# Kernel optimization log

Hardware: AMD Instinct MI355X
Metric: run time of the kernel (lower is better)

Reference implementation:

```python
import jax, jax.numpy as jnp
import numpy as np

C = 768
H = 12
N = 257
B = 64
HID = 4 * C
EPS = 1e-5
SCALE = (C // H) ** -0.5


def layer_norm(x, g, b):
    m = x.mean(-1, keepdims=True)
    v = ((x - m) ** 2).mean(-1, keepdims=True)
    return (x - m) * jax.lax.rsqrt(v + EPS) * g + b


def qkv_split(x, qkv_w):
    # x: [B,N,C]; qkv_w: [3C,C] (torch Linear layout)
    qkv = jnp.einsum('bnc,oc->bno', x, qkv_w)  # [B,N,3C]
    qkv = qkv.reshape(x.shape[0], x.shape[1], 3, H, C // H)
    qkv = jnp.transpose(qkv, (2, 0, 3, 1, 4))  # [3,B,H,N,hd]
    return qkv[0], qkv[1], qkv[2]


def self_attn(x, qkv_w, proj_w, proj_b):
    q, k, v = qkv_split(x, qkv_w)
    attn = jax.nn.softmax(jnp.einsum('bhnd,bhmd->bhnm', q, k) * SCALE, axis=-1)
    o = jnp.einsum('bhnm,bhmd->bhnd', attn, v)
    o = jnp.transpose(o, (0, 2, 1, 3)).reshape(x.shape)
    return jnp.einsum('bnc,oc->bno', o, proj_w) + proj_b


def cross_attn(x, y, qkv_w, proj_w, proj_b):
    qx, _, _ = qkv_split(x, qkv_w)
    _, ky, vy = qkv_split(y, qkv_w)
    attn = jax.nn.softmax(jnp.einsum('bhnd,bhmd->bhnm', qx, ky) * SCALE, axis=-1)
    o = jnp.einsum('bhnm,bhmd->bhnd', attn, vy)
    o = jnp.transpose(o, (0, 2, 1, 3)).reshape(x.shape)
    return jnp.einsum('bnc,oc->bno', o, proj_w) + proj_b, attn.sum(1)  # [B,N,N]


def mlp(x, w1, b1, w2, b2):
    h = jax.nn.gelu(jnp.einsum('bnc,hc->bnh', x, w1) + b1, approximate=False)
    return jnp.einsum('bnh,ch->bnc', h, w2) + b2


def arf(x):
    tmp = (jnp.exp(x) - jnp.exp(-x)) / (jnp.exp(x) + jnp.exp(-x - 4.0))
    return jnp.where(tmp < 0, jnp.zeros_like(x), tmp)


def setup_inputs() -> dict:
    key = jax.random.key(0)
    ks = jax.random.split(key, 16)
    s = 0.02
    return {
        'src': jax.random.normal(ks[0], (B, N, C), jnp.float32),
        'tgt': jax.random.normal(ks[1], (B, N, C), jnp.float32),
        'sattn_qkv_w': jax.random.normal(ks[2], (3 * C, C), jnp.float32) * s,
        'sattn_proj_w': jax.random.normal(ks[3], (C, C), jnp.float32) * s,
        'sattn_proj_b': jnp.zeros((C,), jnp.float32),
        'cattn_qkv_w': jax.random.normal(ks[4], (3 * C, C), jnp.float32) * s,
        'cattn_proj_w': jax.random.normal(ks[5], (C, C), jnp.float32) * s,
        'cattn_proj_b': jnp.zeros((C,), jnp.float32),
        'norm1_g': jnp.ones((C,), jnp.float32),
        'norm1_b': jnp.zeros((C,), jnp.float32),
        'norm2_g': jnp.ones((C,), jnp.float32),
        'norm2_b': jnp.zeros((C,), jnp.float32),
        'fc1_w': jax.random.normal(ks[6], (HID, C), jnp.float32) * s,
        'fc1_b': jnp.zeros((HID,), jnp.float32),
        'fc2_w': jax.random.normal(ks[7], (C, HID), jnp.float32) * s,
        'fc2_b': jnp.zeros((C,), jnp.float32),
        'sa_weight': jnp.ones((1, 1, C), jnp.float32),
        'pos_embed': jax.random.normal(ks[8], (1, N, C), jnp.float32) * s,
    }


def reference(src, tgt, sattn_qkv_w, sattn_proj_w, sattn_proj_b,
              cattn_qkv_w, cattn_proj_w, cattn_proj_b,
              norm1_g, norm1_b, norm2_g, norm2_b,
              fc1_w, fc1_b, fc2_w, fc2_b, sa_weight, pos_embed):
    src = src + pos_embed
    srct = self_attn(layer_norm(src, norm1_g, norm1_b), sattn_qkv_w, sattn_proj_w, sattn_proj_b)
    tgtt = self_attn(layer_norm(tgt, norm1_g, norm1_b), sattn_qkv_w, sattn_proj_w, sattn_proj_b)
    src = src + srct
    tgt = tgt + tgtt
    src = src + mlp(layer_norm(srct, norm2_g, norm2_b), fc1_w, fc1_b, fc2_w, fc2_b)
    tgt = tgt + mlp(layer_norm(tgtt, norm2_g, norm2_b), fc1_w, fc1_b, fc2_w, fc2_b)
    srct, attn_src = cross_attn(layer_norm(src, norm1_g, norm1_b),
                                layer_norm(tgt, norm1_g, norm1_b),
                                cattn_qkv_w, cattn_proj_w, cattn_proj_b)
    srct = arf(srct)
    src = src + srct
    src = src + mlp(layer_norm(srct, norm2_g, norm2_b), fc1_w, fc1_b, fc2_w, fc2_b)
    attm_out = attn_src[:, 1:, 1:]
    # heat gate (no grad through attn_src here)
    heat = jax.lax.stop_gradient(attn_src)
    heat = heat.mean(1).reshape(attn_src.shape[0], N, 1)  # [B,N,1]
    gate = jax.nn.sigmoid(heat)
    tgt = tgt + tgt * sa_weight * gate
    return src, tgt, attm_out
```

## Files before the change

### kernel.cpp

```cpp
#include <hip/hip_runtime.h>

#define N_SEQ  257
#define BATCH  64
#define CDIM   768
#define HEADS  12
#define HDIM   64
#define HIDDEN 3072
#define MROWS  (BATCH * N_SEQ)

typedef unsigned short u16;
typedef unsigned int   u32;
typedef __bf16 bf16x8 __attribute__((ext_vector_type(8)));
typedef float  f32x4  __attribute__((ext_vector_type(4)));

__device__ __forceinline__ float b2f(u16 u) { u32 x = ((u32)u) << 16; return __uint_as_float(x); }
__device__ __forceinline__ u16   f2b(float f) {
    u32 x = __float_as_uint(f);
    u32 r = (x + 0x7fffu + ((x >> 16) & 1u)) >> 16;
    return (u16)r;
}
__device__ __forceinline__ float ldf(const float x) { return x; }
__device__ __forceinline__ float ldf(const u16 x)   { return b2f(x); }

__device__ __forceinline__ float geluf(float x) { return 0.5f * x * (1.f + erff(x * 0.70710678118654752f)); }
__device__ __forceinline__ float arff(float x) {
    if (x <= 0.f) return 0.f;
    float a = expf(-2.f * x);
    float c = expf(-2.f * x - 4.f);
    return (1.f - a) / (1.f + c);
}

template<bool MAXOP>
__device__ __forceinline__ float block_red(float v, float* scratch, int tid) {
#pragma unroll
    for (int off = 32; off > 0; off >>= 1) {
        float o = __shfl_down(v, off, 64);
        v = MAXOP ? fmaxf(v, o) : v + o;
    }
    if ((tid & 63) == 0) scratch[tid >> 6] = v;
    __syncthreads();
    float r = MAXOP ? fmaxf(fmaxf(scratch[0], scratch[1]), fmaxf(scratch[2], scratch[3]))
                    : (scratch[0] + scratch[1]) + (scratch[2] + scratch[3]);
    __syncthreads();
    return r;
}

__global__ void detect_kernel(const u16* __restrict__ g1, u32* __restrict__ flag)
{
    if (threadIdx.x == 0 && blockIdx.x == 0) *flag = (g1[0] == 0x3F80u) ? 1u : 0u;
}

__global__ __launch_bounds__(256)
void conv_kernel(const void* __restrict__ s, u16* __restrict__ d, int n,
                 const u32* __restrict__ flag)
{
    const int i = blockIdx.x * 256 + threadIdx.x;
    if (i >= n) return;
    if (*flag) d[i] = ((const u16*)s)[i];
    else       d[i] = f2b(((const float*)s)[i]);
}

#define LDSW 40

template<int EP>
__global__ __launch_bounds__(256)
void gemm_kernel(const u16* __restrict__ A, const u16* __restrict__ W,
                 const u16* __restrict__ bias, u16* __restrict__ Co,
                 float* __restrict__ resid, int M, int Ncols, int K)
{
    __shared__ __align__(16) u16 sA[128 * LDSW];
    __shared__ __align__(16) u16 sB[128 * LDSW];
    const int tid  = threadIdx.x;
    const int bm0  = blockIdx.y * 128;
    const int n0   = blockIdx.x * 128;
    const int lane = tid & 63, wave = tid >> 6;
    const int wm = (wave >> 1) << 6;
    const int wn = (wave & 1) << 6;
    const int r16 = lane & 15, quad = lane >> 4;

    f32x4 acc[4][4] = {};

    for (int k0 = 0; k0 < K; k0 += 32) {
        __syncthreads();
#pragma unroll
        for (int it = 0; it < 2; ++it) {
            int c2  = tid + (it << 8);
            int row = c2 >> 2;
            int col = (c2 & 3) << 3;
            int gm  = bm0 + row; if (gm >= M) gm = M - 1;
            *reinterpret_cast<uint4*>(&sA[row * LDSW + col]) =
                *reinterpret_cast<const uint4*>(A + (size_t)gm * K + k0 + col);
            *reinterpret_cast<uint4*>(&sB[row * LDSW + col]) =
                *reinterpret_cast<const uint4*>(W + (size_t)(n0 + row) * K + k0 + col);
        }
        __syncthreads();

        bf16x8 af[4], bfr[4];
#pragma unroll
        for (int i = 0; i < 4; ++i) {
            af[i]  = *reinterpret_cast<const bf16x8*>(&sA[(wm + i * 16 + r16) * LDSW + quad * 8]);
            bfr[i] = *reinterpret_cast<const bf16x8*>(&sB[(wn + i * 16 + r16) * LDSW + quad * 8]);
        }
#pragma unroll
        for (int i = 0; i < 4; ++i)
#pragma unroll
            for (int j = 0; j < 4; ++j)
                acc[i][j] = __builtin_amdgcn_mfma_f32_16x16x32_bf16(af[i], bfr[j], acc[i][j], 0, 0, 0);
    }

#pragma unroll
    for (int i = 0; i < 4; ++i) {
#pragma unroll
        for (int j = 0; j < 4; ++j) {
            const int gn = n0 + wn + j * 16 + r16;
            const float bv = bias ? b2f(bias[gn]) : 0.f;
#pragma unroll
            for (int r = 0; r < 4; ++r) {
                const int gm = bm0 + wm + i * 16 + quad * 4 + r;
                if (gm < M) {
                    float v = acc[i][j][r] + bv;
                    const size_t oidx = (size_t)gm * Ncols + gn;
                    if (EP == 1) v = geluf(v);
                    if (EP == 3) v = arff(v);
                    if (EP == 0 || EP == 1) Co[oidx] = f2b(v);
                    if (EP == 2 || EP == 3) { Co[oidx] = f2b(v); resid[oidx] += v; }
                    if (EP == 4) resid[oidx] += v;
                }
            }
        }
    }
}

template<typename T>
__global__ __launch_bounds__(256)
void ln_kernel(const T* __restrict__ x, const u16* __restrict__ g,
               const u16* __restrict__ be, u16* __restrict__ y)
{
    __shared__ float scratch[4];
    const int row = blockIdx.x, tid = threadIdx.x;
    const size_t base = (size_t)row * CDIM;
    float v[3];
#pragma unroll
    for (int i = 0; i < 3; ++i) v[i] = ldf(x[base + tid + i * 256]);
    float mean = block_red<false>(v[0] + v[1] + v[2], scratch, tid) * (1.f / 768.f);
    float d0 = v[0] - mean, d1 = v[1] - mean, d2 = v[2] - mean;
    float var = block_red<false>(d0 * d0 + d1 * d1 + d2 * d2, scratch, tid) * (1.f / 768.f);
    float rstd = rsqrtf(var + 1e-5f);
#pragma unroll
    for (int i = 0; i < 3; ++i) {
        int c = tid + i * 256;
        y[base + c] = f2b((v[i] - mean) * rstd * b2f(g[c]) + b2f(be[c]));
    }
}

__global__ __launch_bounds__(256, 4)
void attn_flash_kernel(const u16* __restrict__ Q, int qs,
                       const u16* __restrict__ Kp, int ks,
                       const u16* __restrict__ Vp, int vs,
                       u16* __restrict__ O,
                       float* __restrict__ Mg, float* __restrict__ Ig)
{
    __shared__ __align__(16) u16 Vt[2][64 * 64];
    __shared__ __align__(16) u16 Ps[64 * 72];
    const int tid = threadIdx.x;
    const int n0 = blockIdx.x * 64;
    const int h  = blockIdx.y, b = blockIdx.z;
    const int lane = tid & 63, w = tid >> 6;
    const int r16 = lane & 15, quad = lane >> 4;

    int qrow = n0 + w * 16 + r16; if (qrow > 256) qrow = 256;
    const u16* qp = Q + (size_t)(b * N_SEQ + qrow) * qs + h * HDIM + quad * 8;
    const bf16x8 af0 = *reinterpret_cast<const bf16x8*>(qp);
    const bf16x8 af1 = *reinterpret_cast<const bf16x8*>(qp + 32);

    auto stageV = [&](int kt, int buf) {
#pragma unroll
        for (int it = 0; it < 2; ++it) {
            int id  = tid + (it << 8);
            int key = id & 63;
            int dc  = ((id >> 6) & 7) << 3;
            int gm  = kt * 64 + key; if (gm > 256) gm = 256;
            uint4 v4 = *reinterpret_cast<const uint4*>(Vp + (size_t)(b * N_SEQ + gm) * vs + h * HDIM + dc);
            const u16* vv = reinterpret_cast<const u16*>(&v4);
#pragma unroll
            for (int j = 0; j < 8; ++j) {
                int d = dc + j;
                Vt[buf][d * 64 + (key ^ ((d & 7) << 3))] = vv[j];
            }
        }
    };

    f32x4 O4[4];
#pragma unroll
    for (int s = 0; s < 4; ++s) O4[s] = (f32x4){0.f, 0.f, 0.f, 0.f};
    float m_[4] = { -3.0e38f, -3.0e38f, -3.0e38f, -3.0e38f };
    float l_[4] = { 0.f, 0.f, 0.f, 0.f };

    stageV(0, 0);
    __syncthreads();

    for (int kt = 0; kt < 5; ++kt) {
        if (kt < 4) stageV(kt + 1, (kt + 1) & 1);

        f32x4 s4[4];
#pragma unroll
        for (int s = 0; s < 4; ++s) s4[s] = (f32x4){0.f, 0.f, 0.f, 0.f};
#pragma unroll
        for (int s = 0; s < 4; ++s) {
            int krow = kt * 64 + s * 16 + r16; if (krow > 256) krow = 256;
            const u16* kp = Kp + (size_t)(b * N_SEQ + krow) * ks + h * HDIM + quad * 8;
            bf16x8 b0 = *reinterpret_cast<const bf16x8*>(kp);
            bf16x8 b1 = *reinterpret_cast<const bf16x8*>(kp + 32);
            s4[s] = __builtin_amdgcn_mfma_f32_16x16x32_bf16(af0, b0, s4[s], 0, 0, 0);
            s4[s] = __builtin_amdgcn_mfma_f32_16x16x32_bf16(af1, b1, s4[s], 0, 0, 0);
        }

#pragma unroll
        for (int s = 0; s < 4; ++s)
#pragma unroll
            for (int r = 0; r < 4; ++r) {
                float v = s4[s][r] * 0.125f;
                if (kt == 4 && (s * 16 + r16) >= 1) v = -3.0e38f;
                s4[s][r] = v;
            }

#pragma unroll
        for (int r = 0; r < 4; ++r) {
            float tmax = fmaxf(fmaxf(s4[0][r], s4[1][r]), fmaxf(s4[2][r], s4[3][r]));
#pragma unroll
            for (int msk = 1; msk < 16; msk <<= 1) tmax = fmaxf(tmax, __shfl_xor(tmax, msk, 64));
            float mn = fmaxf(m_[r], tmax);
            float corr = __expf(m_[r] - mn);
            m_[r] = mn;
            float rs = 0.f;
#pragma unroll
            for (int s = 0; s < 4; ++s) {
                float p = __expf(s4[s][r] - mn);
                s4[s][r] = p; rs += p;
            }
#pragma unroll
            for (int msk = 1; msk < 16; msk <<= 1) rs += __shfl_xor(rs, msk, 64);
            l_[r] = l_[r] * corr + rs;
#pragma unroll
            for (int s = 0; s < 4; ++s) O4[s][r] *= corr;
        }

#pragma unroll
        for (int ts = 0; ts < 4; ++ts)
#pragma unroll
            for (int r = 0; r < 4; ++r)
                Ps[(w * 16 + quad * 4 + r) * 72 + ts * 16 + r16] = f2b(s4[ts][r]);
        bf16x8 p0 = *reinterpret_cast<const bf16x8*>(&Ps[(w * 16 + r16) * 72 + quad * 8]);
        bf16x8 p1 = *reinterpret_cast<const bf16x8*>(&Ps[(w * 16 + r16) * 72 + 32 + quad * 8]);
#pragma unroll
        for (int s = 0; s < 4; ++s) {
            const int d0 = s * 16 + r16;
            const int sw = (d0 & 7) << 3;
            bf16x8 v0 = *reinterpret_cast<const bf16x8*>(&Vt[kt & 1][d0 * 64 + ((quad * 8) ^ sw)]);
            bf16x8 v1 = *reinterpret_cast<const bf16x8*>(&Vt[kt & 1][d0 * 64 + ((32 + quad * 8) ^ sw)]);
            O4[s] = __builtin_amdgcn_mfma_f32_16x16x32_bf16(p0, v0, O4[s], 0, 0, 0);
            O4[s] = __builtin_amdgcn_mfma_f32_16x16x32_bf16(p1, v1, O4[s], 0, 0, 0);
        }

        __syncthreads();
    }

    float inv[4];
#pragma unroll
    for (int r = 0; r < 4; ++r) inv[r] = 1.f / l_[r];

    if (Mg) {
#pragma unroll
        for (int r = 0; r < 4; ++r) {
            const int n = n0 + w * 16 + quad * 4 + r;
            if (r16 == 0 && n < N_SEQ) {
                const size_t mi = (size_t)(b * HEADS + h) * N_SEQ + n;
                Mg[mi] = m_[r]; Ig[mi] = inv[r];
            }
        }
    }

#pragma unroll
    for (int s = 0; s < 4; ++s) {
#pragma unroll
        for (int r = 0; r < 4; ++r) {
            const int n = n0 + w * 16 + quad * 4 + r;
            if (n < N_SEQ)
                O[(size_t)(b * N_SEQ + n) * CDIM + h * HDIM + s * 16 + r16] = f2b(O4[s][r] * inv[r]);
        }
    }
}

__global__ __launch_bounds__(256, 2)
void asum_kernel(const u16* __restrict__ Q, int qs,
                 const u16* __restrict__ Kp, int ks,
                 const float* __restrict__ Mg, const float* __restrict__ Ig,
                 float* __restrict__ asum)
{
    const int tid = threadIdx.x;
    const int n0 = blockIdx.x * 64;
    const int b  = blockIdx.y;
    const int lane = tid & 63, w = tid >> 6;
    const int r16 = lane & 15, quad = lane >> 4;

    f32x4 A00 = {0.f,0.f,0.f,0.f}, A01 = {0.f,0.f,0.f,0.f}, A02 = {0.f,0.f,0.f,0.f}, A03 = {0.f,0.f,0.f,0.f};
    f32x4 A10 = {0.f,0.f,0.f,0.f}, A11 = {0.f,0.f,0.f,0.f}, A12 = {0.f,0.f,0.f,0.f}, A13 = {0.f,0.f,0.f,0.f};
    f32x4 A20 = {0.f,0.f,0.f,0.f}, A21 = {0.f,0.f,0.f,0.f}, A22 = {0.f,0.f,0.f,0.f}, A23 = {0.f,0.f,0.f,0.f};
    f32x4 A30 = {0.f,0.f,0.f,0.f}, A31 = {0.f,0.f,0.f,0.f}, A32 = {0.f,0.f,0.f,0.f}, A33 = {0.f,0.f,0.f,0.f};
    f32x4 A40 = {0.f,0.f,0.f,0.f}, A41 = {0.f,0.f,0.f,0.f}, A42 = {0.f,0.f,0.f,0.f}, A43 = {0.f,0.f,0.f,0.f};

    for (int h = 0; h < HEADS; ++h) {
        int qrow = n0 + w * 16 + r16; if (qrow > 256) qrow = 256;
        const u16* qp = Q + (size_t)(b * N_SEQ + qrow) * qs + h * HDIM + quad * 8;
        const bf16x8 af0 = *reinterpret_cast<const bf16x8*>(qp);
        const bf16x8 af1 = *reinterpret_cast<const bf16x8*>(qp + 32);

        float mv[4], iv[4];
#pragma unroll
        for (int r = 0; r < 4; ++r) {
            int n = n0 + w * 16 + quad * 4 + r; if (n > 256) n = 256;
            const size_t mi = (size_t)(b * HEADS + h) * N_SEQ + n;
            mv[r] = Mg[mi]; iv[r] = Ig[mi];
        }

#define ASUM_TS(KT, S, AV) { \
        int krow = KT * 64 + S * 16 + r16; if (krow > 256) krow = 256; \
        const u16* kp = Kp + (size_t)(b * N_SEQ + krow) * ks + h * HDIM + quad * 8; \
        bf16x8 b0 = *reinterpret_cast<const bf16x8*>(kp); \
        bf16x8 b1 = *reinterpret_cast<const bf16x8*>(kp + 32); \
        f32x4 t = (f32x4){0.f, 0.f, 0.f, 0.f}; \
        t = __builtin_amdgcn_mfma_f32_16x16x32_bf16(af0, b0, t, 0, 0, 0); \
        t = __builtin_amdgcn_mfma_f32_16x16x32_bf16(af1, b1, t, 0, 0, 0); \
        _Pragma("unroll") \
        for (int r = 0; r < 4; ++r) { \
            float p = __expf(t[r] * 0.125f - mv[r]) * iv[r]; \
            if (KT == 4 && (S * 16 + r16) >= 1) p = 0.f; \
            AV[r] += p; \
        } }

        ASUM_TS(0, 0, A00) ASUM_TS(0, 1, A01) ASUM_TS(0, 2, A02) ASUM_TS(0, 3, A03)
        ASUM_TS(1, 0, A10) ASUM_TS(1, 1, A11) ASUM_TS(1, 2, A12) ASUM_TS(1, 3, A13)
        ASUM_TS(2, 0, A20) ASUM_TS(2, 1, A21) ASUM_TS(2, 2, A22) ASUM_TS(2, 3, A23)
        ASUM_TS(3, 0, A30) ASUM_TS(3, 1, A31) ASUM_TS(3, 2, A32) ASUM_TS(3, 3, A33)
        ASUM_TS(4, 0, A40) ASUM_TS(4, 1, A41) ASUM_TS(4, 2, A42) ASUM_TS(4, 3, A43)
#undef ASUM_TS
    }

#define ASUM_ST(KT, S, AV) { \
    _Pragma("unroll") \
    for (int r = 0; r < 4; ++r) { \
        const int n = n0 + w * 16 + quad * 4 + r; \
        const int key = KT * 64 + S * 16 + r16; \
        if (n < N_SEQ && key < N_SEQ) \
            asum[((size_t)b * N_SEQ + n) * N_SEQ + key] = AV[r]; \
    } }

    ASUM_ST(0, 0, A00) ASUM_ST(0, 1, A01) ASUM_ST(0, 2, A02) ASUM_ST(0, 3, A03)
    ASUM_ST(1, 0, A10) ASUM_ST(1, 1, A11) ASUM_ST(1, 2, A12) ASUM_ST(1, 3, A13)
    ASUM_ST(2, 0, A20) ASUM_ST(2, 1, A21) ASUM_ST(2, 2, A22) ASUM_ST(2, 3, A23)
    ASUM_ST(3, 0, A30) ASUM_ST(3, 1, A31) ASUM_ST(3, 2, A32) ASUM_ST(3, 3, A33)
    ASUM_ST(4, 0, A40) ASUM_ST(4, 1, A41) ASUM_ST(4, 2, A42) ASUM_ST(4, 3, A43)
#undef ASUM_ST
}

__global__ __launch_bounds__(256)
void init_kernel(const void* __restrict__ src, const void* __restrict__ tgt,
                 const void* __restrict__ pos, float* __restrict__ sa,
                 float* __restrict__ ta, const u32* __restrict__ flag)
{
    const u32 i = blockIdx.x * 256 + threadIdx.x;
    const u32 p = i % (u32)(N_SEQ * CDIM);
    float sv, tv, pv;
    if (*flag) {
        sv = b2f(((const u16*)src)[i]); tv = b2f(((const u16*)tgt)[i]); pv = b2f(((const u16*)pos)[p]);
    } else {
        sv = ((const float*)src)[i];    tv = ((const float*)tgt)[i];    pv = ((const float*)pos)[p];
    }
    sa[i] = sv + pv;
    ta[i] = tv;
}

__global__ __launch_bounds__(256)
void gate_kernel(const float* __restrict__ asum, float* __restrict__ gate)
{
    const int b = blockIdx.x;
    for (int m = threadIdx.x; m < N_SEQ; m += 256) {
        float s = 0.f;
        for (int q = 0; q < N_SEQ; ++q)
            s += asum[((size_t)b * N_SEQ + q) * N_SEQ + m];
        s *= (1.f / 257.f);
        gate[b * N_SEQ + m] = 1.f / (1.f + expf(-s));
    }
}

__global__ __launch_bounds__(256)
void final_kernel(const float* __restrict__ sa, const float* __restrict__ ta,
                  const u16* __restrict__ saw, const float* __restrict__ gate,
                  void* __restrict__ osrc_v, const u32* __restrict__ flag)
{
    const u32 i = blockIdx.x * 256 + threadIdx.x;
    const int c  = i % CDIM;
    const int bn = i / CDIM;
    const float so = sa[i];
    const float to = ta[i] * (1.f + b2f(saw[c]) * gate[bn]);
    const size_t BNC = (size_t)MROWS * CDIM;
    if (*flag) {
        u16* o = (u16*)osrc_v;
        o[i] = f2b(so); o[BNC + i] = f2b(to);
    } else {
        float* o = (float*)osrc_v;
        o[i] = so; o[BNC + i] = to;
    }
}

__global__ __launch_bounds__(256)
void attm_kernel(const float* __restrict__ asum, void* __restrict__ out_v,
                 const u32* __restrict__ flag)
{
    const u32 i = blockIdx.x * 256 + threadIdx.x;
    const int b = i >> 16;
    const int r = (i >> 8) & 255;
    const int c = i & 255;
    const float v = asum[((size_t)b * N_SEQ + (r + 1)) * N_SEQ + (c + 1)];
    const size_t off = 2 * (size_t)MROWS * CDIM;
    if (*flag) ((u16*)out_v)[off + i] = f2b(v);
    else       ((float*)out_v)[off + i] = v;
}

extern "C" void kernel_launch(void* const* d_in, const int* in_sizes, int n_in,
                              void* d_out, int out_size, void* d_ws, size_t ws_size,
                              hipStream_t stream)
{
    const void* src    = d_in[0];
    const void* tgt    = d_in[1];
    const void* pos    = d_in[17];

    const int M = MROWS;
    const size_t BNC = (size_t)M * CDIM;

    float* SA   = (float*)d_ws;
    float* TA   = SA + BNC;
    u16*   Cb   = (u16*)(TA + BNC);
    u16*   Db   = Cb + BNC;
    u16*   Eb   = Db + BNC;
    float* ASUM = (float*)(Eb + 4 * BNC);
    float* GATE = ASUM + (size_t)BATCH * N_SEQ * N_SEQ;
    u16*   WB   = (u16*)(GATE + (size_t)BATCH * N_SEQ);
    u16* w_sqkv   = WB;
    u16* w_sproj  = w_sqkv  + 1769472;
    u16* w_sprojb = w_sproj + 589824;
    u16* w_cqkv   = w_sprojb + 768;
    u16* w_cproj  = w_cqkv  + 1769472;
    u16* w_cprojb = w_cproj + 589824;
    u16* w_g1     = w_cprojb + 768;
    u16* w_b1     = w_g1 + 768;
    u16* w_g2     = w_b1 + 768;
    u16* w_b2     = w_g2 + 768;
    u16* w_fc1    = w_b2 + 768;
    u16* w_fc1b   = w_fc1 + 2359296;
    u16* w_fc2    = w_fc1b + 3072;
    u16* w_fc2b   = w_fc2 + 2359296;
    u16* w_saw    = w_fc2b + 768;
    u32* FLAG     = (u32*)(w_saw + 768);
    const size_t NMI = (size_t)BATCH * HEADS * N_SEQ;
    float* MG     = (float*)(FLAG + 4);
    float* IG     = MG + NMI;
    if (ws_size < (size_t)((char*)(IG + NMI) - (char*)d_ws)) return;

    const dim3 blk(256, 1, 1);
    const int gM = (M + 127) / 128;
    const dim3 agrid(5, HEADS, BATCH);

    detect_kernel<<<dim3(1), dim3(64), 0, stream>>>((const u16*)d_in[8], FLAG);

    auto conv = [&](int idx, u16* dst, int n) {
        conv_kernel<<<dim3((n + 255) / 256), blk, 0, stream>>>(d_in[idx], dst, n, FLAG);
    };
    conv(2,  w_sqkv,   1769472);
    conv(3,  w_sproj,  589824);
    conv(4,  w_sprojb, 768);
    conv(5,  w_cqkv,   1769472);
    conv(6,  w_cproj,  589824);
    conv(7,  w_cprojb, 768);
    conv(8,  w_g1,     768);
    conv(9,  w_b1,     768);
    conv(10, w_g2,     768);
    conv(11, w_b2,     768);
    conv(12, w_fc1,    2359296);
    conv(13, w_fc1b,   3072);
    conv(14, w_fc2,    2359296);
    conv(15, w_fc2b,   768);
    conv(16, w_saw,    768);

    init_kernel<<<dim3((u32)(BNC / 256)), blk, 0, stream>>>(src, tgt, pos, SA, TA, FLAG);

    ln_kernel<float><<<dim3(M), blk, 0, stream>>>(SA, w_g1, w_b1, Db);
    gemm_kernel<0><<<dim3(2304 / 128, gM), blk, 0, stream>>>(Db, w_sqkv, nullptr, Eb, nullptr, M, 2304, CDIM);
    attn_flash_kernel<<<agrid, blk, 0, stream>>>(Eb, 2304, Eb + 768, 2304, Eb + 1536, 2304, Db, nullptr, nullptr);
    gemm_kernel<2><<<dim3(6, gM), blk, 0, stream>>>(Db, w_sproj, w_sprojb, Cb, SA, M, CDIM, CDIM);
    ln_kernel<u16><<<dim3(M), blk, 0, stream>>>(Cb, w_g2, w_b2, Db);
    gemm_kernel<1><<<dim3(HIDDEN / 128, gM), blk, 0, stream>>>(Db, w_fc1, w_fc1b, Eb, nullptr, M, HIDDEN, CDIM);
    gemm_kernel<4><<<dim3(6, gM), blk, 0, stream>>>(Eb, w_fc2, w_fc2b, nullptr, SA, M, CDIM, HIDDEN);

    ln_kernel<float><<<dim3(M), blk, 0, stream>>>(TA, w_g1, w_b1, Db);
    gemm_kernel<0><<<dim3(2304 / 128, gM), blk, 0, stream>>>(Db, w_sqkv, nullptr, Eb, nullptr, M, 2304, CDIM);
    attn_flash_kernel<<<agrid, blk, 0, stream>>>(Eb, 2304, Eb + 768, 2304, Eb + 1536, 2304, Db, nullptr, nullptr);
    gemm_kernel<2><<<dim3(6, gM), blk, 0, stream>>>(Db, w_sproj, w_sprojb, Cb, TA, M, CDIM, CDIM);
    ln_kernel<u16><<<dim3(M), blk, 0, stream>>>(Cb, w_g2, w_b2, Db);
    gemm_kernel<1><<<dim3(HIDDEN / 128, gM), blk, 0, stream>>>(Db, w_fc1, w_fc1b, Eb, nullptr, M, HIDDEN, CDIM);
    gemm_kernel<4><<<dim3(6, gM), blk, 0, stream>>>(Eb, w_fc2, w_fc2b, nullptr, TA, M, CDIM, HIDDEN);

    u16* EKV = Eb + BNC;
    ln_kernel<float><<<dim3(M), blk, 0, stream>>>(SA, w_g1, w_b1, Db);
    gemm_kernel<0><<<dim3(6, gM), blk, 0, stream>>>(Db, w_cqkv, nullptr, Eb, nullptr, M, CDIM, CDIM);
    ln_kernel<float><<<dim3(M), blk, 0, stream>>>(TA, w_g1, w_b1, Db);
    gemm_kernel<0><<<dim3(12, gM), blk, 0, stream>>>(Db, w_cqkv + 768 * 768, nullptr, EKV, nullptr, M, 1536, CDIM);
    attn_flash_kernel<<<agrid, blk, 0, stream>>>(Eb, 768, EKV, 1536, EKV + 768, 1536, Db, MG, IG);
    asum_kernel<<<dim3(5, BATCH), blk, 0, stream>>>(Eb, 768, EKV, 1536, MG, IG, ASUM);
    gemm_kernel<3><<<dim3(6, gM), blk, 0, stream>>>(Db, w_cproj, w_cprojb, Cb, SA, M, CDIM, CDIM);
    ln_kernel<u16><<<dim3(M), blk, 0, stream>>>(Cb, w_g2, w_b2, Db);
    gemm_kernel<1><<<dim3(HIDDEN / 128, gM), blk, 0, stream>>>(Db, w_fc1, w_fc1b, Eb, nullptr, M, HIDDEN, CDIM);
    gemm_kernel<4><<<dim3(6, gM), blk, 0, stream>>>(Eb, w_fc2, w_fc2b, nullptr, SA, M, CDIM, HIDDEN);

    gate_kernel<<<dim3(BATCH), blk, 0, stream>>>(ASUM, GATE);
    final_kernel<<<dim3((u32)(BNC / 256)), blk, 0, stream>>>(SA, TA, w_saw, GATE, d_out, FLAG);
    attm_kernel<<<dim3(BATCH * 256 * 256 / 256), blk, 0, stream>>>(ASUM, d_out, FLAG);
}
```

Baseline: 2.523 ms.

## Double-buffer GEMM LDS tiles with register prefetch and XCD-aware block swizzle

The GEMM main loop now keeps two LDS buffers. The next K-slice's global loads are issued into registers before the MFMA block and written to the alternate buffer afterward, so memory latency overlaps compute and one barrier per iteration is dropped. Workgroup IDs are remapped so consecutive tiles land on the same XCD, which is meant to improve L2 reuse of shared A/W rows. LDS use doubles and register pressure rises from the prefetch registers, which may reduce occupancy.

```diff
diff --git a/kernel.cpp b/kernel.cpp
--- a/kernel.cpp
+++ b/kernel.cpp
@@ -30,6 +30,13 @@
     return (1.f - a) / (1.f + c);
 }
 
+__device__ __forceinline__ u32 xcd_swz(u32 orig, u32 nwg) {
+    u32 xcd = orig & 7u;
+    u32 q = nwg >> 3, r = nwg & 7u;
+    u32 base = (xcd < r) ? xcd * (q + 1u) : r * (q + 1u) + (xcd - r) * q;
+    return base + (orig >> 3);
+}
+
 template<bool MAXOP>
 __device__ __forceinline__ float block_red(float v, float* scratch, int tid) {
 #pragma unroll
@@ -68,44 +75,69 @@
                  const u16* __restrict__ bias, u16* __restrict__ Co,
                  float* __restrict__ resid, int M, int Ncols, int K)
 {
-    __shared__ __align__(16) u16 sA[128 * LDSW];
-    __shared__ __align__(16) u16 sB[128 * LDSW];
+    __shared__ __align__(16) u16 sA[2][128 * LDSW];
+    __shared__ __align__(16) u16 sB[2][128 * LDSW];
     const int tid  = threadIdx.x;
-    const int bm0  = blockIdx.y * 128;
-    const int n0   = blockIdx.x * 128;
+    const u32 nwg  = gridDim.x * gridDim.y;
+    const u32 wg   = xcd_swz(blockIdx.y * gridDim.x + blockIdx.x, nwg);
+    const int n0   = (int)(wg % gridDim.x) * 128;
+    const int bm0  = (int)(wg / gridDim.x) * 128;
     const int lane = tid & 63, wave = tid >> 6;
     const int wm = (wave >> 1) << 6;
     const int wn = (wave & 1) << 6;
     const int r16 = lane & 15, quad = lane >> 4;
 
+    const int row0 = tid >> 2,        col0 = (tid & 3) << 3;
+    const int row1 = (tid + 256) >> 2;
+    int gmA0 = bm0 + row0; if (gmA0 >= M) gmA0 = M - 1;
+    int gmA1 = bm0 + row1; if (gmA1 >= M) gmA1 = M - 1;
+    const u16* pA0 = A + (size_t)gmA0 * K + col0;
+    const u16* pA1 = A + (size_t)gmA1 * K + col0;
+    const u16* pW0 = W + (size_t)(n0 + row0) * K + col0;
+    const u16* pW1 = W + (size_t)(n0 + row1) * K + col0;
+
     f32x4 acc[4][4] = {};
 
-    for (int k0 = 0; k0 < K; k0 += 32) {
-        __syncthreads();
-#pragma unroll
-        for (int it = 0; it < 2; ++it) {
-            int c2  = tid + (it << 8);
-            int row = c2 >> 2;
-            int col = (c2 & 3) << 3;
-            int gm  = bm0 + row; if (gm >= M) gm = M - 1;
-            *reinterpret_cast<uint4*>(&sA[row * LDSW + col]) =
-                *reinterpret_cast<const uint4*>(A + (size_t)gm * K + k0 + col);
-            *reinterpret_cast<uint4*>(&sB[row * LDSW + col]) =
-                *reinterpret_cast<const uint4*>(W + (size_t)(n0 + row) * K + k0 + col);
-        }
-        __syncthreads();
+    *reinterpret_cast<uint4*>(&sA[0][row0 * LDSW + col0]) = *reinterpret_cast<const uint4*>(pA0);
+    *reinterpret_cast<uint4*>(&sA[0][row1 * LDSW + col0]) = *reinterpret_cast<const uint4*>(pA1);
+    *reinterpret_cast<uint4*>(&sB[0][row0 * LDSW + col0]) = *reinterpret_cast<const uint4*>(pW0);
+    *reinterpret_cast<uint4*>(&sB[0][row1 * LDSW + col0]) = *reinterpret_cast<const uint4*>(pW1);
+    __syncthreads();
+
+    const int nk = K >> 5;
+    for (int ik = 0; ik < nk; ++ik) {
+        const int cur = ik & 1;
 
         bf16x8 af[4], bfr[4];
 #pragma unroll
         for (int i = 0; i < 4; ++i) {
-            af[i]  = *reinterpret_cast<const bf16x8*>(&sA[(wm + i * 16 + r16) * LDSW + quad * 8]);
-            bfr[i] = *reinterpret_cast<const bf16x8*>(&sB[(wn + i * 16 + r16) * LDSW + quad * 8]);
-        }
+            af[i]  = *reinterpret_cast<const bf16x8*>(&sA[cur][(wm + i * 16 + r16) * LDSW + quad * 8]);
+            bfr[i] = *reinterpret_cast<const bf16x8*>(&sB[cur][(wn + i * 16 + r16) * LDSW + quad * 8]);
+        }
+
+        uint4 ra0, ra1, rb0, rb1;
+        const bool pf = (ik + 1 < nk);
+        if (pf) {
+            const int k1 = (ik + 1) << 5;
+            ra0 = *reinterpret_cast<const uint4*>(pA0 + k1);
+            ra1 = *reinterpret_cast<const uint4*>(pA1 + k1);
+            rb0 = *reinterpret_cast<const uint4*>(pW0 + k1);
+            rb1 = *reinterpret_cast<const uint4*>(pW1 + k1);
+        }
+
 #pragma unroll
         for (int i = 0; i < 4; ++i)
 #pragma unroll
             for (int j = 0; j < 4; ++j)
                 acc[i][j] = __builtin_amdgcn_mfma_f32_16x16x32_bf16(af[i], bfr[j], acc[i][j], 0, 0, 0);
+
+        if (pf) {
+            *reinterpret_cast<uint4*>(&sA[cur ^ 1][row0 * LDSW + col0]) = ra0;
+            *reinterpret_cast<uint4*>(&sA[cur ^ 1][row1 * LDSW + col0]) = ra1;
+            *reinterpret_cast<uint4*>(&sB[cur ^ 1][row0 * LDSW + col0]) = rb0;
+            *reinterpret_cast<uint4*>(&sB[cur ^ 1][row1 * LDSW + col0]) = rb1;
+        }
+        __syncthreads();
     }
 
 #pragma unroll
```

After: 2.339 ms. 1.08x faster.
